# Performance work log

Measured on AMD Instinct MI355X. Metric: run time of the kernel, lower is better.

The kernel has to match this reference:

```python
import math
import jax, jax.numpy as jnp
from jax import lax
import numpy as np

TWO_PI = 2.0 * math.pi
CG_ITERS = 30      # DifferentiableLinearSolver(max_iter=30)
CG_TOL = 1e-6
CG_REG = 1e-6      # reg = 1e-6 * I added inside the solver


def build_second_diff_matrix(N, dtype):
    e = jnp.ones(N, dtype)
    e2 = -2.0 * e
    e2 = e2.at[0].set(-1.0).at[-1].set(-1.0)
    oper = jnp.diag(e2) + jnp.diag(e[:-1], -1) + jnp.diag(e[:-1], 1)
    return oper.T @ oper


def cumtrapz(y, dx):
    # cumulative trapezoid along last axis, keeping length (leading zero)
    avg = (y[..., :-1] + y[..., 1:]) * (0.5 * dx)
    c = jnp.cumsum(avg, axis=-1)
    return jnp.concatenate([jnp.zeros_like(y[..., :1]), c], axis=-1)


def differ5(y, delta):
    mid = (y[..., 2:] - y[..., :-2]) / (2.0 * delta)
    first = (y[..., 1:2] - y[..., 0:1]) / delta
    last = (y[..., -1:] - y[..., -2:-1]) / delta
    return jnp.concatenate([first, mid, last], axis=-1)


def projec5(vec, var):
    # per-row norm-ball projection; vec: (B, N)
    M = vec.shape[-1]
    e = jnp.sqrt(M * var)
    n = jnp.linalg.norm(vec, axis=-1, keepdims=True)
    scale = jnp.where(n > e, e / jnp.maximum(n, 1e-30), 1.0)
    return vec * scale


def cg_solve(opedoub, coef, diagv, rhs, x0):
    # Solves (coef*opedoub + diag(diagv) + CG_REG*I) x = rhs via CG,
    # matching torch semantics (early break freezes state).
    def mv(p):
        return coef * (opedoub @ p) + (diagv + CG_REG) * p

    r0 = rhs - mv(x0)
    rs0 = jnp.dot(r0, r0)

    def step(carry, _):
        x, r, p, rsold, done = carry
        Ap = mv(p)
        a = rsold / (jnp.dot(p, Ap) + 1e-12)
        x1 = jnp.where(done, x, x + a * p)
        r1 = jnp.where(done, r, r - a * Ap)
        rsnew = jnp.dot(r1, r1)
        done1 = done | (jnp.sqrt(rsnew) < CG_TOL)
        bta = rsnew / (rsold + 1e-12)
        p1 = jnp.where(done1, p, r1 + bta * p)
        rsold1 = jnp.where(done1, rsold, rsnew)
        return (x1, r1, p1, rsold1, done1), None

    (x, _, _, _, _), _ = lax.scan(step, (x0, r0, r0, rs0, jnp.array(False)), None, length=CG_ITERS)
    return x


def _forward(s, eIF, xm, ym, sum_x, sum_y, lamuda, init_freqs, mode_mask,
             alpha, beta, var, fs, iteration,
             fe_w1, fe_b1, fe_w2, fe_b2,
             pr_w1, pr_b1, pr_w2, pr_b2, pr_w3, pr_b3, iter_weight):
    dtype = s.dtype
    B, N = s.shape
    K = eIF.shape[1]

    # ---- hyperparameter refinement MLP ----
    avg = jnp.mean(init_freqs, axis=1, keepdims=True)              # (B,1)
    h = jax.nn.relu(avg @ fe_w1.T + fe_b1)
    h = jax.nn.relu(h @ fe_w2.T + fe_b2)                            # (B,16)
    cur = jnp.stack([jnp.broadcast_to(alpha, (B,)),
                     jnp.broadcast_to(beta, (B,))], axis=1)         # (B,2)
    z = jnp.concatenate([h, cur], axis=1)                           # (B,18)
    z = jax.nn.relu(z @ pr_w1.T + pr_b1)
    z = jax.nn.relu(z @ pr_w2.T + pr_b2)
    res = jnp.tanh(z @ pr_w3.T + pr_b3)                             # (B,2)
    fac = jax.nn.sigmoid(iter_weight * iteration)
    res = res * fac * 0.1
    new_alpha = jnp.clip(alpha + jnp.mean(res[:, 0] * alpha), 1e-6, 0.01)
    new_beta = jnp.clip(beta + jnp.mean(res[:, 1] * beta), 1e-6, 0.1)

    betathr = jnp.minimum(10.0 ** (iteration / 36.0 - 10.0), new_beta)
    opedoub = build_second_diff_matrix(N, dtype)
    dx = 1.0 / fs

    # Within the torch k-loop, temp sums / lamuda / new_eIF[b,k] all still hold
    # their *input* values, so all (b,k) sub-problems are independent -> vmap.
    u = projec5(s - sum_x - sum_y - lamuda / new_alpha, var)        # (B,N)

    phase = TWO_PI * cumtrapz(eIF, dx)                               # (B,K,N)
    cosm = jnp.cos(phase)
    sinm = jnp.sin(phase)
    resid = (s[:, None, :] - (sum_x[:, None, :] - xm * cosm)
             - (sum_y[:, None, :] - ym * sinm)
             - u[:, None, :] - (lamuda / new_alpha)[:, None, :])
    rhs_x = cosm * resid
    rhs_y = sinm * resid

    coefA = 2.0 / new_alpha
    flat = lambda t: t.reshape(B * K, N)
    cg_v = jax.vmap(cg_solve, in_axes=(None, None, 0, 0, 0))

    xs = cg_v(opedoub, coefA, flat(cosm ** 2), flat(rhs_x), flat(xm)).reshape(B, K, N)
    ys = cg_v(opedoub, coefA, flat(sinm ** 2), flat(rhs_y), flat(ym)).reshape(B, K, N)

    xbar = differ5(xs, dx)
    ybar = differ5(ys, dx)
    denom = xs ** 2 + ys ** 2 + 1e-12
    deltaIF = (xs * ybar - ys * xbar) / (denom * TWO_PI)

    coefS = 2.0 / betathr
    ones_d = jnp.ones((B * K, N), dtype)
    zeros_d = jnp.zeros((B * K, N), dtype)
    smooth = cg_v(opedoub, coefS, ones_d, flat(deltaIF), zeros_d).reshape(B, K, N)
    eIF_s = eIF - 0.5 * smooth

    active = (mode_mask != 0)[:, :, None]                            # (B,K,1)
    new_xm = jnp.where(active, xs, xm)
    new_ym = jnp.where(active, ys, ym)
    new_eIF = jnp.where(active, eIF_s, eIF)

    new_phase = TWO_PI * cumtrapz(new_eIF, dx)
    maskf = active.astype(dtype)
    bsx = jnp.sum(maskf * new_xm * jnp.cos(new_phase), axis=1)       # (B,N)
    bsy = jnp.sum(maskf * new_ym * jnp.sin(new_phase), axis=1)
    new_lamuda = lamuda + new_alpha * (u + bsx + bsy - s)

    return (new_eIF, new_xm, new_ym, bsx, bsy, new_lamuda, new_alpha, new_beta)


def setup_inputs() -> dict:
    key = jax.random.key(0)
    B, K, N = 8, 4, 2048
    ks = jax.random.split(key, 20)
    f32 = jnp.float32
    inp = {
        "s": jax.random.normal(ks[0], (B, N), f32),
        "eIF": 50.0 + 200.0 * jax.random.uniform(ks[1], (B, K, N), f32),
        "xm": 0.1 * jax.random.normal(ks[2], (B, K, N), f32),
        "ym": 0.1 * jax.random.normal(ks[3], (B, K, N), f32),
        "sum_x": 0.1 * jax.random.normal(ks[4], (B, N), f32),
        "sum_y": 0.1 * jax.random.normal(ks[5], (B, N), f32),
        "lamuda": 0.01 * jax.random.normal(ks[6], (B, N), f32),
        "init_freqs": 50.0 + 200.0 * jax.random.uniform(ks[7], (B, K), f32),
        "mode_mask": jnp.ones((B, K), jnp.int32),
        "alpha": jnp.asarray(0.005, f32),
        "beta": jnp.asarray(0.05, f32),
        "var": jnp.asarray(0.01, f32),
        "fs": jnp.asarray(2000.0, f32),
        "iteration": 1,
        # HyperparameterRefinement params (torch Linear: y = x @ W.T + b)
        "fe_w1": 0.1 * jax.random.normal(ks[8], (32, 1), f32),
        "fe_b1": jnp.zeros((32,), f32),
        "fe_w2": 0.1 * jax.random.normal(ks[9], (16, 32), f32),
        "fe_b2": jnp.zeros((16,), f32),
        "pr_w1": 0.1 * jax.random.normal(ks[10], (64, 18), f32),
        "pr_b1": jnp.zeros((64,), f32),
        "pr_w2": 0.1 * jax.random.normal(ks[11], (32, 64), f32),
        "pr_b2": jnp.zeros((32,), f32),
        "pr_w3": 0.1 * jax.random.normal(ks[12], (2, 32), f32),
        "pr_b3": jnp.zeros((2,), f32),
        "iter_weight": jnp.asarray(0.1, f32),
    }
    return inp


def reference(s, eIF, xm, ym, sum_x, sum_y, lamuda, init_freqs, mode_mask,
              alpha, beta, var, fs, iteration,
              fe_w1, fe_b1, fe_w2, fe_b2,
              pr_w1, pr_b1, pr_w2, pr_b2, pr_w3, pr_b3, iter_weight):
    return _forward(s, eIF, xm, ym, sum_x, sum_y, lamuda, init_freqs, mode_mask,
                    alpha, beta, var, fs, iteration,
                    fe_w1, fe_b1, fe_w2, fe_b2,
                    pr_w1, pr_b1, pr_w2, pr_b2, pr_w3, pr_b3, iter_weight)
```

## Files before the change

### kernel.cpp

```cpp
#include <hip/hip_runtime.h>
#include <math.h>

#define Nq 2048
#define Bq 8
#define Kq 4
#define BKq 32
#define NL 32
#define NP 16
#define TWO_PI_D 6.283185307179586
#define PI_D 3.141592653589793
#define INV2PI_D 0.15915494309189535

typedef float v2f __attribute__((ext_vector_type(2)));

__device__ __forceinline__ v2f mk2(float a, float b) {
  v2f r; r.x = a; r.y = b; return r;
}


__device__ __forceinline__ double wave_sum_d(double v) {
#pragma unroll
  for (int off = 1; off < 64; off <<= 1) v += __shfl_xor(v, off, 64);
  return v;
}

__device__ __forceinline__ float dpp_sum_f32(float v) {
  v += __int_as_float(__builtin_amdgcn_update_dpp(0, __float_as_int(v), 0x111, 0xf, 0xf, false));
  v += __int_as_float(__builtin_amdgcn_update_dpp(0, __float_as_int(v), 0x112, 0xf, 0xf, false));
  v += __int_as_float(__builtin_amdgcn_update_dpp(0, __float_as_int(v), 0x114, 0xf, 0xe, false));
  v += __int_as_float(__builtin_amdgcn_update_dpp(0, __float_as_int(v), 0x118, 0xf, 0xc, false));
  v += __int_as_float(__builtin_amdgcn_update_dpp(0, __float_as_int(v), 0x142, 0xa, 0xf, false));
  v += __int_as_float(__builtin_amdgcn_update_dpp(0, __float_as_int(v), 0x143, 0xc, 0xf, false));
  return __int_as_float(__builtin_amdgcn_readlane(__float_as_int(v), 63));
}

__device__ __forceinline__ float dpp_shr1(float v) {
  return __int_as_float(__builtin_amdgcn_update_dpp(0, __float_as_int(v), 0x138, 0xf, 0xf, false));
}
__device__ __forceinline__ float dpp_shl1(float v) {
  return __int_as_float(__builtin_amdgcn_update_dpp(0, __float_as_int(v), 0x130, 0xf, 0xf, false));
}

__device__ __forceinline__ double lane_excl_prefix_d(double T, int lane) {
  double acc = T;
#pragma unroll
  for (int off = 1; off < 64; off <<= 1) {
    double t = __shfl_up(acc, off, 64);
    if (lane >= off) acc += t;
  }
  return acc - T;
}

__device__ __forceinline__ void fast_sincos_ph(double ph, float* sn, float* cs) {
  double k = trunc(ph * INV2PI_D);
  float phr = (float)(ph - k * TWO_PI_D);
  __sincosf(phr, sn, cs);
}

template <bool UNIT_DIAG, bool ZERO_X0>
__device__ __forceinline__ void cg_wave_pk(float coef, const v2f* De, float deu,
                                           v2f* R, v2f* X, int lane) {
  v2f P[NP], AP[NP];

  auto applyA = [&](const v2f* V) {
    float lm2 = dpp_shr1(V[NP - 1].x);
    float lm1 = dpp_shr1(V[NP - 1].y);
    float rp1 = dpp_shl1(V[0].x);
    float rp2 = dpp_shl1(V[0].y);
    v2f Vm = mk2(lm2, lm1);
    v2f Vp = mk2(rp1, rp2);
#pragma unroll
    for (int j = 0; j < NP; ++j) {
      v2f Vprev = (j == 0) ? Vm : V[j - 1];
      v2f Vnext = (j == NP - 1) ? Vp : V[j + 1];
      v2f t = Vprev + Vnext;
      t += V[j] * 6.0f;
      float m1x = Vprev.y + V[j].y;
      float m1y = V[j].x + Vnext.x;
      t.x -= 4.0f * m1x;
      t.y -= 4.0f * m1y;
      v2f de = UNIT_DIAG ? mk2(deu, deu) : De[j];
      AP[j] = t * coef + de * V[j];
    }
    if (lane == 0) {
      float p0 = V[0].x, p1 = V[0].y, p2 = V[1].x, p3 = V[1].y;
      float d0 = UNIT_DIAG ? deu : De[0].x;
      float d1 = UNIT_DIAG ? deu : De[0].y;
      AP[0].x = coef * (2.0f * p0 - 3.0f * p1 + p2) + d0 * p0;
      AP[0].y = coef * (-3.0f * p0 + 6.0f * p1 - 4.0f * p2 + p3) + d1 * p1;
    }
    if (lane == 63) {
      float q0 = V[NP - 2].x, q1 = V[NP - 2].y, q2 = V[NP - 1].x, q3 = V[NP - 1].y;
      float d0 = UNIT_DIAG ? deu : De[NP - 1].x;
      float d1 = UNIT_DIAG ? deu : De[NP - 1].y;
      AP[NP - 1].x = coef * (q0 - 4.0f * q1 + 6.0f * q2 - 3.0f * q3) + d0 * q2;
      AP[NP - 1].y = coef * (q1 - 3.0f * q2 + 2.0f * q3) + d1 * q3;
    }
  };

  float rsold;
  {
    if (!ZERO_X0) {
      applyA(X);
#pragma unroll
      for (int j = 0; j < NP; ++j) R[j] -= AP[j];
    }
    v2f a0 = mk2(0.f, 0.f), a1 = mk2(0.f, 0.f);
#pragma unroll
    for (int j = 0; j < NP; j += 2) {
      P[j] = R[j];
      a0 += R[j] * R[j];
      P[j + 1] = R[j + 1];
      a1 += R[j + 1] * R[j + 1];
    }
    v2f s = a0 + a1;
    rsold = dpp_sum_f32(s.x + s.y);
  }

  for (int it = 0; it < 30; ++it) {
    applyA(P);
    v2f a0 = mk2(0.f, 0.f), a1 = mk2(0.f, 0.f);
#pragma unroll
    for (int j = 0; j < NP; j += 2) {
      a0 += P[j] * AP[j];
      a1 += P[j + 1] * AP[j + 1];
    }
    v2f s = a0 + a1;
    float pap = dpp_sum_f32(s.x + s.y);
    float a = rsold * __builtin_amdgcn_rcpf(pap + 1e-12f);
    v2f r0 = mk2(0.f, 0.f), r1 = mk2(0.f, 0.f);
#pragma unroll
    for (int j = 0; j < NP; j += 2) {
      X[j] += P[j] * a;
      R[j] -= AP[j] * a;
      r0 += R[j] * R[j];
      X[j + 1] += P[j + 1] * a;
      R[j + 1] -= AP[j + 1] * a;
      r1 += R[j + 1] * R[j + 1];
    }
    v2f t = r0 + r1;
    float rsnew = dpp_sum_f32(t.x + t.y);
    if (rsnew < 1e-12f) break;
    float bta = rsnew * __builtin_amdgcn_rcpf(rsold + 1e-12f);
#pragma unroll
    for (int j = 0; j < NP; ++j) P[j] = R[j] + P[j] * bta;
    rsold = rsnew;
  }
}

__device__ __forceinline__ double blk_reduce(double v, double* sh) {
#pragma unroll
  for (int off = 32; off > 0; off >>= 1) v += __shfl_down(v, off, 64);
  int wid = threadIdx.x >> 6;
  int lane = threadIdx.x & 63;
  __syncthreads();
  if (lane == 0) sh[wid] = v;
  __syncthreads();
  double r = sh[0] + sh[1] + sh[2] + sh[3];
  __syncthreads();
  return r;
}

__global__ __launch_bounds__(128, 1) void row_kernel(
    const float* __restrict__ s, const float* __restrict__ eIF,
    const float* __restrict__ xm, const float* __restrict__ ym,
    const float* __restrict__ sum_x, const float* __restrict__ sum_y,
    const float* __restrict__ lamuda, const float* __restrict__ init_freqs,
    const int* __restrict__ mode_mask, const float* __restrict__ alpha_p,
    const float* __restrict__ beta_p, const float* __restrict__ var_p,
    const float* __restrict__ fs_p, const int* __restrict__ iter_p,
    const float* __restrict__ fe_w1, const float* __restrict__ fe_b1,
    const float* __restrict__ fe_w2, const float* __restrict__ fe_b2,
    const float* __restrict__ pr_w1, const float* __restrict__ pr_b1,
    const float* __restrict__ pr_w2, const float* __restrict__ pr_b2,
    const float* __restrict__ pr_w3, const float* __restrict__ pr_b3,
    const float* __restrict__ iter_w_p, double* __restrict__ hdr,
    float* __restrict__ out_eIF, float* __restrict__ out_xm,
    float* __restrict__ out_ym, float* __restrict__ cx_w,
    float* __restrict__ cy_w, float* __restrict__ out_scal) {
  __shared__ double sh_avg[Bq];
  __shared__ double sh_h1[Bq][32];
  __shared__ double sh_z[Bq][18];
  __shared__ double sh_z1[Bq][64];
  __shared__ double sh_z2[Bq][32];
  __shared__ double sh_res[Bq][2];
  __shared__ double sh_hdr[6];
  __shared__ float sh_xs[Nq], sh_ys[Nq];

  const int tid = threadIdx.x;
  const int wv = tid >> 6, lane = tid & 63;
  const int row = blockIdx.x, b = row >> 2;
  const int bb = b * Nq, base = row * Nq;

  double alpha = (double)alpha_p[0], beta = (double)beta_p[0];
  double iterv = (double)iter_p[0];
  if (tid < Bq) {
    double avg = 0.0;
#pragma unroll
    for (int k = 0; k < Kq; ++k) avg += (double)init_freqs[tid * Kq + k];
    sh_avg[tid] = avg * (1.0 / Kq);
  }
  __syncthreads();
  for (int n = tid; n < 256; n += 128) {
    int b2 = n >> 5, j = n & 31;
    double v = (double)fe_w1[j] * sh_avg[b2] + (double)fe_b1[j];
    sh_h1[b2][j] = v > 0.0 ? v : 0.0;
  }
  __syncthreads();
  {
    int b2 = tid >> 4, j = tid & 15;
    double acc = (double)fe_b2[j];
    for (int i = 0; i < 32; ++i) acc += (double)fe_w2[j * 32 + i] * sh_h1[b2][i];
    sh_z[b2][j] = acc > 0.0 ? acc : 0.0;
  }
  if (tid < Bq) {
    sh_z[tid][16] = alpha;
    sh_z[tid][17] = beta;
  }
  __syncthreads();
  for (int n = tid; n < 512; n += 128) {
    int b2 = n >> 6, j = n & 63;
    double acc = (double)pr_b1[j];
    for (int i = 0; i < 18; ++i) acc += (double)pr_w1[j * 18 + i] * sh_z[b2][i];
    sh_z1[b2][j] = acc > 0.0 ? acc : 0.0;
  }
  __syncthreads();
  for (int n = tid; n < 256; n += 128) {
    int b2 = n >> 5, j = n & 31;
    double acc = (double)pr_b2[j];
    for (int i = 0; i < 64; ++i) acc += (double)pr_w2[j * 64 + i] * sh_z1[b2][i];
    sh_z2[b2][j] = acc > 0.0 ? acc : 0.0;
  }
  __syncthreads();
  if (tid < 16) {
    int b2 = tid >> 1, c = tid & 1;
    double acc = (double)pr_b3[c];
    for (int i = 0; i < 32; ++i) acc += (double)pr_w3[c * 32 + i] * sh_z2[b2][i];
    double fac = 1.0 / (1.0 + exp(-(double)iter_w_p[0] * iterv));
    sh_res[b2][c] = tanh(acc) * fac * 0.1;
  }
  __syncthreads();
  if (tid == 0) {
    double r0 = 0.0, r1 = 0.0;
    for (int q = 0; q < Bq; ++q) { r0 += sh_res[q][0]; r1 += sh_res[q][1]; }
    double na = fmin(fmax(alpha + r0 * alpha * (1.0 / Bq), 1e-6), 0.01);
    double nb = fmin(fmax(beta + r1 * beta * (1.0 / Bq), 1e-6), 0.1);
    double betathr = fmin(pow(10.0, iterv / 36.0 - 10.0), nb);
    sh_hdr[0] = na;
    sh_hdr[1] = 2.0 / na;
    sh_hdr[2] = 2.0 / betathr;
    sh_hdr[3] = 1.0 / na;
    hdr[0] = na;
    hdr[4] = 1.0 / na;
    out_scal[0] = (float)na;
    out_scal[1] = (float)nb;
  }
  __syncthreads();
  const float coefA = (float)sh_hdr[1];
  const float coefS = (float)sh_hdr[2];
  const double inva = sh_hdr[3];

  double tv[NL];
  {
    double n0 = 0.0, n1 = 0.0;
#pragma unroll
    for (int e = 0; e < NL; ++e) {
      int gi = bb + lane * NL + e;
      tv[e] = (double)s[gi] - (double)sum_x[gi] - (double)sum_y[gi] -
              (double)lamuda[gi] * inva;
      ((e & 1) ? n1 : n0) += tv[e] * tv[e];
    }
    double nsq = wave_sum_d(n0 + n1);
    double nn = sqrt(nsq);
    double ee = sqrt((double)Nq * (double)var_p[0]);
    double scale = (nn > ee) ? ee / fmax(nn, 1e-30) : 1.0;
    double oms = 1.0 - scale;
#pragma unroll
    for (int e = 0; e < NL; ++e) tv[e] *= oms;
  }

  const double dx = 1.0 / (double)fs_p[0];
  const double c0 = PI_D * dx;
  v2f De[NP], R[NP], X[NP];
  {
    double ev[NL], pl[NL];
#pragma unroll
    for (int e = 0; e < NL; ++e) ev[e] = (double)eIF[base + lane * NL + e];
    pl[0] = ev[0];
#pragma unroll
    for (int e = 1; e < NL; ++e) pl[e] = pl[e - 1] + ev[e];
    double offs = lane_excl_prefix_d(pl[NL - 1], lane);
    double y0 = __shfl(ev[0], 0, 64);
#pragma unroll
    for (int e = 0; e < NL; ++e) {
      int i = lane * NL + e;
      double ph = c0 * (2.0 * (offs + pl[e]) - ev[e] - y0);
      float sn, cs;
      fast_sincos_ph(ph, &sn, &cs);
      float xmv = xm[base + i], ymv = ym[base + i];
      double resid = tv[e] + (double)xmv * (double)cs + (double)ymv * (double)sn;
      float trig = (wv == 0) ? cs : sn;
      float de = trig * trig + 1e-6f;
      float rr = (float)((double)trig * resid);
      float xx = (wv == 0) ? xmv : ymv;
      int j = e >> 1;
      if (e & 1) {
        De[j].y = de; R[j].y = rr; X[j].y = xx;
      } else {
        De[j].x = de; R[j].x = rr; X[j].x = xx;
      }
    }
  }

  cg_wave_pk<false, false>(coefA, De, 0.0f, R, X, lane);

  {
    float* dst = (wv == 0) ? sh_xs : sh_ys;
#pragma unroll
    for (int e = 0; e < NL; ++e) {
      float xv = (e & 1) ? X[e >> 1].y : X[e >> 1].x;
      dst[e * 64 + lane] = xv;
    }
  }
  __syncthreads();

  {
    float xs[NL], ys[NL];
#pragma unroll
    for (int e = 0; e < NL; ++e) {
      xs[e] = sh_xs[e * 64 + lane];
      ys[e] = sh_ys[e * 64 + lane];
    }
    float invdx = (float)fs_p[0], inv2dx = 0.5f * invdx;
    float xl = dpp_shr1(xs[NL - 1]), xr = dpp_shl1(xs[0]);
    float yl = dpp_shr1(ys[NL - 1]), yr = dpp_shl1(ys[0]);
#pragma unroll
    for (int e = 0; e < NL; ++e) {
      int i = lane * NL + e;
      float xm1 = (e >= 1) ? xs[e - 1] : xl;
      float xp1 = (e <= NL - 2) ? xs[e + 1] : xr;
      float ym1 = (e >= 1) ? ys[e - 1] : yl;
      float yp1 = (e <= NL - 2) ? ys[e + 1] : yr;
      float xb, yb;
      if (i == 0) {
        xb = (xp1 - xs[e]) * invdx;
        yb = (yp1 - ys[e]) * invdx;
      } else if (i == Nq - 1) {
        xb = (xs[e] - xm1) * invdx;
        yb = (ys[e] - ym1) * invdx;
      } else {
        xb = (xp1 - xm1) * inv2dx;
        yb = (yp1 - ym1) * inv2dx;
      }
      float denom = xs[e] * xs[e] + ys[e] * ys[e] + 1e-12f;
      float rr = (xs[e] * yb - ys[e] * xb) / (denom * (float)TWO_PI_D);
      int j = e >> 1;
      if (e & 1) {
        R[j].y = rr; X[j].y = 0.0f;
      } else {
        R[j].x = rr; X[j].x = 0.0f;
      }
    }
  }

  cg_wave_pk<true, true>(coefS, nullptr, 1.0f + 1e-6f, R, X, lane);

  bool active = mode_mask[row] != 0;
  double eifn[NL], pl[NL];
#pragma unroll
  for (int e = 0; e < NL; ++e) {
    int i = base + lane * NL + e;
    double eifv = (double)eIF[i];
    double sm = (double)((e & 1) ? X[e >> 1].y : X[e >> 1].x);
    eifn[e] = active ? (eifv - 0.5 * sm) : eifv;
  }
  if (wv == 0) {
#pragma unroll
    for (int e = 0; e < NL; ++e) {
      int i = base + lane * NL + e;
      out_eIF[i] = (float)eifn[e];
      out_xm[i] = active ? sh_xs[e * 64 + lane] : xm[i];
    }
  } else {
#pragma unroll
    for (int e = 0; e < NL; ++e) {
      int i = base + lane * NL + e;
      out_ym[i] = active ? sh_ys[e * 64 + lane] : ym[i];
    }
  }
  pl[0] = eifn[0];
#pragma unroll
  for (int e = 1; e < NL; ++e) pl[e] = pl[e - 1] + eifn[e];
  double offs = lane_excl_prefix_d(pl[NL - 1], lane);
  double y0 = __shfl(eifn[0], 0, 64);
#pragma unroll
  for (int e = 0; e < NL; ++e) {
    int i = base + lane * NL + e;
    double ph = c0 * (2.0 * (offs + pl[e]) - eifn[e] - y0);
    float sn, cs;
    fast_sincos_ph(ph, &sn, &cs);
    if (wv == 0)
      cx_w[i] = active ? sh_xs[e * 64 + lane] * cs : 0.0f;
    else
      cy_w[i] = active ? sh_ys[e * 64 + lane] * sn : 0.0f;
  }
}

__global__ __launch_bounds__(256) void final_kernel(
    const float* __restrict__ s, const float* __restrict__ sum_x,
    const float* __restrict__ sum_y, const float* __restrict__ lamuda,
    const float* __restrict__ var_p, const double* __restrict__ hdr,
    const float* __restrict__ cx_w, const float* __restrict__ cy_w,
    float* __restrict__ out_bsx, float* __restrict__ out_bsy,
    float* __restrict__ out_lam) {
  __shared__ double sh_red[4];
  __shared__ double sh_scale;
  int b = blockIdx.x;
  int bb = b * Nq;
  int tid = threadIdx.x;
  double na = hdr[0], inva = hdr[4];
  double t[8];
  double loc = 0.0;
#pragma unroll
  for (int e = 0; e < 8; ++e) {
    int gi = bb + tid + e * 256;
    t[e] = (double)s[gi] - (double)sum_x[gi] - (double)sum_y[gi] -
           (double)lamuda[gi] * inva;
    loc += t[e] * t[e];
  }
  double nsq = blk_reduce(loc, sh_red);
  if (tid == 0) {
    double n = sqrt(nsq);
    double ee = sqrt((double)Nq * (double)var_p[0]);
    sh_scale = (n > ee) ? ee / fmax(n, 1e-30) : 1.0;
  }
  __syncthreads();
  double scale = sh_scale;
#pragma unroll
  for (int e = 0; e < 8; ++e) {
    int i = tid + e * 256;
    int gi = bb + i;
    double bx = 0.0, by = 0.0;
#pragma unroll
    for (int k = 0; k < Kq; ++k) {
      bx += (double)cx_w[(b * Kq + k) * Nq + i];
      by += (double)cy_w[(b * Kq + k) * Nq + i];
    }
    double u = t[e] * scale;
    double nl = (double)lamuda[gi] + na * (u + bx + by - (double)s[gi]);
    out_bsx[gi] = (float)bx;
    out_bsy[gi] = (float)by;
    out_lam[gi] = (float)nl;
  }
}

extern "C" void kernel_launch(void* const* d_in, const int* in_sizes, int n_in,
                              void* d_out, int out_size, void* d_ws, size_t ws_size,
                              hipStream_t stream) {
  (void)in_sizes; (void)n_in; (void)out_size; (void)ws_size;
  const float* s = (const float*)d_in[0];
  const float* eIF = (const float*)d_in[1];
  const float* xm = (const float*)d_in[2];
  const float* ym = (const float*)d_in[3];
  const float* sum_x = (const float*)d_in[4];
  const float* sum_y = (const float*)d_in[5];
  const float* lamuda = (const float*)d_in[6];
  const float* init_freqs = (const float*)d_in[7];
  const int* mode_mask = (const int*)d_in[8];
  const float* alpha = (const float*)d_in[9];
  const float* beta = (const float*)d_in[10];
  const float* var = (const float*)d_in[11];
  const float* fs = (const float*)d_in[12];
  const int* iteration = (const int*)d_in[13];
  const float* fe_w1 = (const float*)d_in[14];
  const float* fe_b1 = (const float*)d_in[15];
  const float* fe_w2 = (const float*)d_in[16];
  const float* fe_b2 = (const float*)d_in[17];
  const float* pr_w1 = (const float*)d_in[18];
  const float* pr_b1 = (const float*)d_in[19];
  const float* pr_w2 = (const float*)d_in[20];
  const float* pr_b2 = (const float*)d_in[21];
  const float* pr_w3 = (const float*)d_in[22];
  const float* pr_b3 = (const float*)d_in[23];
  const float* iter_weight = (const float*)d_in[24];

  float* out = (float*)d_out;
  const int BN = Bq * Nq;
  const int BKN = BKq * Nq;
  float* out_eIF = out;
  float* out_xm = out + BKN;
  float* out_ym = out + 2 * BKN;
  float* out_bsx = out + 3 * BKN;
  float* out_bsy = out + 3 * BKN + BN;
  float* out_lam = out + 3 * BKN + 2 * BN;
  float* out_scal = out + 3 * BKN + 3 * BN;

  double* W = (double*)d_ws;
  double* hdr = W;
  float* F = (float*)(W + 16);
  float* cx_w = F;
  float* cy_w = F + BKN;

  row_kernel<<<BKq, 128, 0, stream>>>(
      s, eIF, xm, ym, sum_x, sum_y, lamuda, init_freqs, mode_mask, alpha, beta,
      var, fs, iteration, fe_w1, fe_b1, fe_w2, fe_b2, pr_w1, pr_b1, pr_w2,
      pr_b2, pr_w3, pr_b3, iter_weight, hdr, out_eIF, out_xm, out_ym, cx_w,
      cy_w, out_scal);
  final_kernel<<<Bq, 256, 0, stream>>>(s, sum_x, sum_y, lamuda, var, hdr, cx_w,
                                       cy_w, out_bsx, out_bsy, out_lam);
}
```

Measured before the change: 164.2 us.

## Vectorize row loads, reuse row scale in final kernel, simplify CG boundary

Row kernel loads s, sum_x, sum_y, lamuda, eIF, xm and ym as float4 instead of scalar loads. It also stores the per-row projection scale into the header so the final kernel no longer recomputes the norm with a block reduction. The final kernel becomes a flat elementwise kernel with many more 128-thread blocks. The CG boundary correction becomes an additive fixup, and the reciprocal of rsold is computed ahead of the beta update. The main risk is the rewritten boundary formula for the band matrix, which must match the original exactly.

```diff
diff --git a/kernel.cpp b/kernel.cpp
--- a/kernel.cpp
+++ b/kernel.cpp
@@ -83,22 +83,16 @@
       AP[j] = t * coef + de * V[j];
     }
     if (lane == 0) {
-      float p0 = V[0].x, p1 = V[0].y, p2 = V[1].x, p3 = V[1].y;
-      float d0 = UNIT_DIAG ? deu : De[0].x;
-      float d1 = UNIT_DIAG ? deu : De[0].y;
-      AP[0].x = coef * (2.0f * p0 - 3.0f * p1 + p2) + d0 * p0;
-      AP[0].y = coef * (-3.0f * p0 + 6.0f * p1 - 4.0f * p2 + p3) + d1 * p1;
+      AP[0].x += coef * (V[0].y - 4.0f * V[0].x);
+      AP[0].y += coef * V[0].x;
     }
     if (lane == 63) {
-      float q0 = V[NP - 2].x, q1 = V[NP - 2].y, q2 = V[NP - 1].x, q3 = V[NP - 1].y;
-      float d0 = UNIT_DIAG ? deu : De[NP - 1].x;
-      float d1 = UNIT_DIAG ? deu : De[NP - 1].y;
-      AP[NP - 1].x = coef * (q0 - 4.0f * q1 + 6.0f * q2 - 3.0f * q3) + d0 * q2;
-      AP[NP - 1].y = coef * (q1 - 3.0f * q2 + 2.0f * q3) + d1 * q3;
+      AP[NP - 1].x += coef * V[NP - 1].y;
+      AP[NP - 1].y += coef * (V[NP - 1].x - 4.0f * V[NP - 1].y);
     }
   };
 
-  float rsold;
+  float rsold, inv_rsold;
   {
     if (!ZERO_X0) {
       applyA(X);
@@ -115,6 +109,7 @@
     }
     v2f s = a0 + a1;
     rsold = dpp_sum_f32(s.x + s.y);
+    inv_rsold = __builtin_amdgcn_rcpf(rsold + 1e-12f);
   }
 
   for (int it = 0; it < 30; ++it) {
@@ -141,24 +136,12 @@
     v2f t = r0 + r1;
     float rsnew = dpp_sum_f32(t.x + t.y);
     if (rsnew < 1e-12f) break;
-    float bta = rsnew * __builtin_amdgcn_rcpf(rsold + 1e-12f);
+    float bta = rsnew * inv_rsold;
 #pragma unroll
     for (int j = 0; j < NP; ++j) P[j] = R[j] + P[j] * bta;
     rsold = rsnew;
-  }
-}
-
-__device__ __forceinline__ double blk_reduce(double v, double* sh) {
-#pragma unroll
-  for (int off = 32; off > 0; off >>= 1) v += __shfl_down(v, off, 64);
-  int wid = threadIdx.x >> 6;
-  int lane = threadIdx.x & 63;
-  __syncthreads();
-  if (lane == 0) sh[wid] = v;
-  __syncthreads();
-  double r = sh[0] + sh[1] + sh[2] + sh[3];
-  __syncthreads();
-  return r;
+    inv_rsold = __builtin_amdgcn_rcpf(rsnew + 1e-12f);
+  }
 }
 
 __global__ __launch_bounds__(128, 1) void row_kernel(
@@ -262,18 +245,32 @@
 
   double tv[NL];
   {
+    const float4* S4 = reinterpret_cast<const float4*>(s + bb);
+    const float4* SX4 = reinterpret_cast<const float4*>(sum_x + bb);
+    const float4* SY4 = reinterpret_cast<const float4*>(sum_y + bb);
+    const float4* L4 = reinterpret_cast<const float4*>(lamuda + bb);
     double n0 = 0.0, n1 = 0.0;
 #pragma unroll
-    for (int e = 0; e < NL; ++e) {
-      int gi = bb + lane * NL + e;
-      tv[e] = (double)s[gi] - (double)sum_x[gi] - (double)sum_y[gi] -
-              (double)lamuda[gi] * inva;
-      ((e & 1) ? n1 : n0) += tv[e] * tv[e];
+    for (int q = 0; q < 8; ++q) {
+      float4 av = S4[lane * 8 + q];
+      float4 bv = SX4[lane * 8 + q];
+      float4 cv = SY4[lane * 8 + q];
+      float4 dv = L4[lane * 8 + q];
+      int e = 4 * q;
+      tv[e + 0] = (double)av.x - (double)bv.x - (double)cv.x - (double)dv.x * inva;
+      tv[e + 1] = (double)av.y - (double)bv.y - (double)cv.y - (double)dv.y * inva;
+      tv[e + 2] = (double)av.z - (double)bv.z - (double)cv.z - (double)dv.z * inva;
+      tv[e + 3] = (double)av.w - (double)bv.w - (double)cv.w - (double)dv.w * inva;
+      n0 += tv[e + 0] * tv[e + 0];
+      n1 += tv[e + 1] * tv[e + 1];
+      n0 += tv[e + 2] * tv[e + 2];
+      n1 += tv[e + 3] * tv[e + 3];
     }
     double nsq = wave_sum_d(n0 + n1);
     double nn = sqrt(nsq);
     double ee = sqrt((double)Nq * (double)var_p[0]);
     double scale = (nn > ee) ? ee / fmax(nn, 1e-30) : 1.0;
+    if (tid == 0 && (row & 3) == 0) hdr[8 + b] = scale;
     double oms = 1.0 - scale;
 #pragma unroll
     for (int e = 0; e < NL; ++e) tv[e] *= oms;
@@ -284,30 +281,46 @@
   v2f De[NP], R[NP], X[NP];
   {
     double ev[NL], pl[NL];
-#pragma unroll
-    for (int e = 0; e < NL; ++e) ev[e] = (double)eIF[base + lane * NL + e];
+    const float4* E4 = reinterpret_cast<const float4*>(eIF + base);
+#pragma unroll
+    for (int q = 0; q < 8; ++q) {
+      float4 e4 = E4[lane * 8 + q];
+      ev[4 * q + 0] = (double)e4.x;
+      ev[4 * q + 1] = (double)e4.y;
+      ev[4 * q + 2] = (double)e4.z;
+      ev[4 * q + 3] = (double)e4.w;
+    }
     pl[0] = ev[0];
 #pragma unroll
     for (int e = 1; e < NL; ++e) pl[e] = pl[e - 1] + ev[e];
     double offs = lane_excl_prefix_d(pl[NL - 1], lane);
     double y0 = __shfl(ev[0], 0, 64);
-#pragma unroll
-    for (int e = 0; e < NL; ++e) {
-      int i = lane * NL + e;
-      double ph = c0 * (2.0 * (offs + pl[e]) - ev[e] - y0);
-      float sn, cs;
-      fast_sincos_ph(ph, &sn, &cs);
-      float xmv = xm[base + i], ymv = ym[base + i];
-      double resid = tv[e] + (double)xmv * (double)cs + (double)ymv * (double)sn;
-      float trig = (wv == 0) ? cs : sn;
-      float de = trig * trig + 1e-6f;
-      float rr = (float)((double)trig * resid);
-      float xx = (wv == 0) ? xmv : ymv;
-      int j = e >> 1;
-      if (e & 1) {
-        De[j].y = de; R[j].y = rr; X[j].y = xx;
-      } else {
-        De[j].x = de; R[j].x = rr; X[j].x = xx;
+    const float4* XM4 = reinterpret_cast<const float4*>(xm + base);
+    const float4* YM4 = reinterpret_cast<const float4*>(ym + base);
+#pragma unroll
+    for (int q = 0; q < 8; ++q) {
+      float4 xm4 = XM4[lane * 8 + q];
+      float4 ym4 = YM4[lane * 8 + q];
+      float xa[4] = {xm4.x, xm4.y, xm4.z, xm4.w};
+      float ya[4] = {ym4.x, ym4.y, ym4.z, ym4.w};
+#pragma unroll
+      for (int t2 = 0; t2 < 4; ++t2) {
+        int e = 4 * q + t2;
+        double ph = c0 * (2.0 * (offs + pl[e]) - ev[e] - y0);
+        float sn, cs;
+        fast_sincos_ph(ph, &sn, &cs);
+        float xmv = xa[t2], ymv = ya[t2];
+        double resid = tv[e] + (double)xmv * (double)cs + (double)ymv * (double)sn;
+        float trig = (wv == 0) ? cs : sn;
+        float de = trig * trig + 1e-6f;
+        float rr = (float)((double)trig * resid);
+        float xx = (wv == 0) ? xmv : ymv;
+        int j = e >> 1;
+        if (e & 1) {
+          De[j].y = de; R[j].y = rr; X[j].y = xx;
+        } else {
+          De[j].x = de; R[j].x = rr; X[j].x = xx;
+        }
       }
     }
   }
@@ -406,52 +419,29 @@
   }
 }
 
-__global__ __launch_bounds__(256) void final_kernel(
+__global__ __launch_bounds__(128) void final_kernel(
     const float* __restrict__ s, const float* __restrict__ sum_x,
     const float* __restrict__ sum_y, const float* __restrict__ lamuda,
-    const float* __restrict__ var_p, const double* __restrict__ hdr,
-    const float* __restrict__ cx_w, const float* __restrict__ cy_w,
-    float* __restrict__ out_bsx, float* __restrict__ out_bsy,
-    float* __restrict__ out_lam) {
-  __shared__ double sh_red[4];
-  __shared__ double sh_scale;
-  int b = blockIdx.x;
-  int bb = b * Nq;
-  int tid = threadIdx.x;
-  double na = hdr[0], inva = hdr[4];
-  double t[8];
-  double loc = 0.0;
-#pragma unroll
-  for (int e = 0; e < 8; ++e) {
-    int gi = bb + tid + e * 256;
-    t[e] = (double)s[gi] - (double)sum_x[gi] - (double)sum_y[gi] -
-           (double)lamuda[gi] * inva;
-    loc += t[e] * t[e];
-  }
-  double nsq = blk_reduce(loc, sh_red);
-  if (tid == 0) {
-    double n = sqrt(nsq);
-    double ee = sqrt((double)Nq * (double)var_p[0]);
-    sh_scale = (n > ee) ? ee / fmax(n, 1e-30) : 1.0;
-  }
-  __syncthreads();
-  double scale = sh_scale;
-#pragma unroll
-  for (int e = 0; e < 8; ++e) {
-    int i = tid + e * 256;
-    int gi = bb + i;
-    double bx = 0.0, by = 0.0;
-#pragma unroll
-    for (int k = 0; k < Kq; ++k) {
-      bx += (double)cx_w[(b * Kq + k) * Nq + i];
-      by += (double)cy_w[(b * Kq + k) * Nq + i];
-    }
-    double u = t[e] * scale;
-    double nl = (double)lamuda[gi] + na * (u + bx + by - (double)s[gi]);
-    out_bsx[gi] = (float)bx;
-    out_bsy[gi] = (float)by;
-    out_lam[gi] = (float)nl;
-  }
+    const double* __restrict__ hdr, const float* __restrict__ cx_w,
+    const float* __restrict__ cy_w, float* __restrict__ out_bsx,
+    float* __restrict__ out_bsy, float* __restrict__ out_lam) {
+  int gi = blockIdx.x * 128 + threadIdx.x;
+  int b = gi >> 11, i = gi & (Nq - 1);
+  double na = hdr[0], inva = hdr[4], scale = hdr[8 + b];
+  double sv = (double)s[gi];
+  double t = sv - (double)sum_x[gi] - (double)sum_y[gi] -
+             (double)lamuda[gi] * inva;
+  double bx = 0.0, by = 0.0;
+#pragma unroll
+  for (int k = 0; k < Kq; ++k) {
+    bx += (double)cx_w[(b * Kq + k) * Nq + i];
+    by += (double)cy_w[(b * Kq + k) * Nq + i];
+  }
+  double u = t * scale;
+  double nl = (double)lamuda[gi] + na * (u + bx + by - sv);
+  out_bsx[gi] = (float)bx;
+  out_bsy[gi] = (float)by;
+  out_lam[gi] = (float)nl;
 }
 
 extern "C" void kernel_launch(void* const* d_in, const int* in_sizes, int n_in,
@@ -506,6 +496,7 @@
       var, fs, iteration, fe_w1, fe_b1, fe_w2, fe_b2, pr_w1, pr_b1, pr_w2,
       pr_b2, pr_w3, pr_b3, iter_weight, hdr, out_eIF, out_xm, out_ym, cx_w,
       cy_w, out_scal);
-  final_kernel<<<Bq, 256, 0, stream>>>(s, sum_x, sum_y, lamuda, var, hdr, cx_w,
-                                       cy_w, out_bsx, out_bsy, out_lam);
-}
+  final_kernel<<<BN / 128, 128, 0, stream>>>(s, sum_x, sum_y, lamuda, hdr,
+                                             cx_w, cy_w, out_bsx, out_bsy,
+                                             out_lam);
+}
```

After: 158.8 us. -3.2%, faster.
